# Kernel tuning notes

Measured on AMD Instinct MI355X. Metric: run time of the kernel, lower is better.

Reference implementation:

```python
import jax, jax.numpy as jnp
import numpy as np
from jax import lax

B, S, F, H, A, C = 256, 128, 128, 512, 512, 128


def _gru_cell(x, h, Wih, Whh, bih, bhh):
    # PyTorch GRU cell: gates ordered (r, z, n)
    gi = x @ Wih.T + bih            # [B, 3H]
    gh = h @ Whh.T + bhh            # [B, 3H]
    ir, iz, inn = jnp.split(gi, 3, axis=-1)
    hr, hz, hn = jnp.split(gh, 3, axis=-1)
    r = jax.nn.sigmoid(ir + hr)
    z = jax.nn.sigmoid(iz + hz)
    n = jnp.tanh(inn + r * hn)
    return (1.0 - z) * n + z * h


def setup_inputs() -> dict:
    key = jax.random.key(0)
    ks = jax.random.split(key, 13)
    def n(k, shape, s=0.05):
        return jax.random.normal(k, shape, dtype=jnp.float32) * s
    return dict(
        x=n(ks[0], (B, S, F), 1.0),
        y=jax.random.randint(ks[1], (B, C), 0, S),
        enc_Wih=n(ks[2], (3 * H, F)), enc_Whh=n(ks[3], (3 * H, H)),
        enc_bih=n(ks[4], (3 * H,)), enc_bhh=n(ks[5], (3 * H,)),
        dec_Wih=n(ks[6], (3 * H, F)), dec_Whh=n(ks[7], (3 * H, H)),
        dec_bih=n(ks[8], (3 * H,)), dec_bhh=n(ks[9], (3 * H,)),
        w1=n(ks[10], (A, H)), w2=n(ks[11], (A, H)), v=n(ks[12], (A,)),
    )


def reference(x, y, enc_Wih, enc_Whh, enc_bih, enc_bhh,
              dec_Wih, dec_Whh, dec_bih, dec_bhh, w1, w2, v):
    b, s, f = x.shape
    c = y.shape[1]
    h0 = jnp.zeros((b, H), x.dtype)

    # ---- encoder GRU over sequence ----
    def enc_step(h, xt):
        h2 = _gru_cell(xt, h, enc_Wih, enc_Whh, enc_bih, enc_bhh)
        return h2, h2
    hT, enc_out = lax.scan(enc_step, h0, jnp.swapaxes(x, 0, 1))  # enc_out [S,B,H]
    enc_out = jnp.swapaxes(enc_out, 0, 1)                        # [B,S,H]

    # w1(enc_out) is loop-invariant: precompute (same math as recomputing per step)
    enc_proj = jnp.einsum('bsh,ah->bsa', enc_out, w1)            # [B,S,A]

    # ---- decoder pointer loop (teacher_force_ratio=0.0 -> always use argmax) ----
    def dec_step(carry, y_i):
        h, dec_in = carry
        h = _gru_cell(dec_in, h, dec_Wih, dec_Whh, dec_bih, dec_bhh)  # [B,H]
        att = jax.nn.relu(enc_proj + (h @ w2.T)[:, None, :])          # [B,S,A]
        prob = jax.nn.softmax(jnp.einsum('bsa,a->bs', att, v), axis=1)  # [B,S]
        # faithful to original: F.cross_entropy applied to probabilities
        logp = jax.nn.log_softmax(prob, axis=1)
        step_loss = -jnp.mean(jnp.take_along_axis(logp, y_i[:, None], axis=1))
        pred = jnp.argmax(prob, axis=1)                               # [B]
        dec_in_next = jnp.take_along_axis(x, pred[:, None, None], axis=1)[:, 0, :]
        return (h, dec_in_next), (pred, step_loss)

    dec_in0 = jnp.zeros((b, f), x.dtype)
    (_, _), (preds, losses) = lax.scan(dec_step, (hT, dec_in0), y.T)
    preds = preds.T                                   # [B, C]
    loss = jnp.sum(losses) / b / c
    return preds, loss
```

## Files before the change

kernel.cpp:

```cpp
#include <hip/hip_runtime.h>
#include <math.h>

#define B_ 256
#define S_ 128
#define F_ 128
#define H_ 512
#define A_ 512
#define C_ 128

#define DOT4(va, vb) ((va).x*(vb).x + (va).y*(vb).y + (va).z*(vb).z + (va).w*(vb).w)

__global__ __launch_bounds__(256)
void transpose_x(const float* __restrict__ x, float* __restrict__ xT)
{
    const int t = blockIdx.x >> 2;
    const int f0 = (blockIdx.x & 3) * 32;
    const int b = threadIdx.x;
#pragma unroll 4
    for (int ff = 0; ff < 32; ++ff) {
        int f = f0 + ff;
        xT[(size_t)t * (F_ * B_) + (size_t)f * B_ + b] =
            x[(size_t)b * (S_ * F_) + (size_t)t * F_ + f];
    }
}

__global__ __launch_bounds__(256)
void prep_w6(const float* __restrict__ Wih, const float* __restrict__ Whh,
             float* __restrict__ W6)
{
    int id = blockIdx.x * 256 + threadIdx.x;
    if (id >= 256 * 640 * 6) return;
    int up = id / 3840;
    int rem = id - up * 3840;
    int k = rem / 6, g = rem - k * 6;
    int row = (g >> 1) * H_ + up * 2 + (g & 1);
    float val;
    if (k < F_) val = Wih[(size_t)row * F_ + k];
    else        val = Whh[(size_t)row * H_ + (k - F_)];
    W6[id] = val;
}

__global__ __launch_bounds__(256)
void prep_w2q(const float* __restrict__ w2, float4* __restrict__ w2q,
              float* __restrict__ dec_inT)
{
    int id = blockIdx.x * 256 + threadIdx.x;
    if (id < 128 * 512) {
        int k4 = id >> 9, a = id & 511;
        const float* s = w2 + (size_t)a * H_ + k4 * 4;
        w2q[id] = make_float4(s[0], s[1], s[2], s[3]);
    }
    if (id < F_ * B_) dec_inT[id] = 0.f;
}

__global__ __launch_bounds__(256)
void prep_bias(const float* __restrict__ ebih, const float* __restrict__ ebhh,
               const float* __restrict__ dbih, const float* __restrict__ dbhh,
               float* __restrict__ bias4e, float* __restrict__ bias4d,
               float* __restrict__ h0T)
{
    int id = blockIdx.x * 256 + threadIdx.x;
    if (id < H_ * B_) h0T[id] = 0.f;
    if (id < H_) {
        bias4e[id * 4 + 0] = ebih[id] + ebhh[id];
        bias4e[id * 4 + 1] = ebih[H_ + id] + ebhh[H_ + id];
        bias4e[id * 4 + 2] = ebih[2 * H_ + id];
        bias4e[id * 4 + 3] = ebhh[2 * H_ + id];
        bias4d[id * 4 + 0] = dbih[id] + dbhh[id];
        bias4d[id * 4 + 1] = dbih[H_ + id] + dbhh[H_ + id];
        bias4d[id * 4 + 2] = dbih[2 * H_ + id];
        bias4d[id * 4 + 3] = dbhh[2 * H_ + id];
    }
}

template<int NH>
__device__ __forceinline__ void acc_range(const float* __restrict__ src,
                                          const float* __restrict__ W6k,
                                          int nk, int b, float* __restrict__ acc)
{
    float a0[8], a1[8];
#pragma unroll
    for (int j = 0; j < 8; ++j) a0[j] = src[(size_t)j * B_ + b];
    for (int kc = 0; kc < nk; kc += 8) {
        if (kc + 8 < nk) {
#pragma unroll
            for (int j = 0; j < 8; ++j) a1[j] = src[(size_t)(kc + 8 + j) * B_ + b];
        }
        const float* Wr = W6k + (size_t)kc * 6;
#pragma unroll
        for (int j = 0; j < 8; ++j) {
            float av = a0[j];
            acc[0]      = fmaf(av, Wr[j * 6 + 0], acc[0]);
            acc[1]      = fmaf(av, Wr[j * 6 + 1], acc[1]);
            acc[2]      = fmaf(av, Wr[j * 6 + 2], acc[2]);
            acc[3]      = fmaf(av, Wr[j * 6 + 3], acc[3]);
            acc[NH]     = fmaf(av, Wr[j * 6 + 4], acc[NH]);
            acc[NH + 1] = fmaf(av, Wr[j * 6 + 5], acc[NH + 1]);
        }
#pragma unroll
        for (int j = 0; j < 8; ++j) a0[j] = a1[j];
    }
}

__global__ __launch_bounds__(512)
void gru_step(const float* __restrict__ inT,
              const float* __restrict__ hinT,
              const float* __restrict__ W6,
              const float* __restrict__ bias4,
              float* __restrict__ houtT,
              float* __restrict__ hB)
{
    __shared__ float accL[256][6];
    const int tid = threadIdx.x;
    const int lane = tid & 63;
    const int w = tid >> 6;
    const int bg = w & 3;
    const int kw = w >> 2;
    const int b = bg * 64 + lane;
    const int up = blockIdx.x;
    const float* Wb = W6 + (size_t)up * (640 * 6);

    float acc[8];
#pragma unroll
    for (int g = 0; g < 8; ++g) acc[g] = 0.f;

    if (kw == 0) {
        acc_range<4>(inT, Wb, F_, b, acc);
        acc_range<6>(hinT, Wb + F_ * 6, 192, b, acc);
    } else {
        acc_range<6>(hinT + (size_t)192 * B_, Wb + 320 * 6, 320, b, acc);
    }

    if (kw == 1) {
        const int li = tid & 255;
        accL[li][0] = acc[0]; accL[li][1] = acc[1];
        accL[li][2] = acc[2]; accL[li][3] = acc[3];
        accL[li][4] = acc[6]; accL[li][5] = acc[7];
    }
    __syncthreads();
    if (kw == 0) {
        const int u0 = up * 2, u1 = u0 + 1;
        float4 bb0 = *(const float4*)(bias4 + u0 * 4);
        float4 bb1 = *(const float4*)(bias4 + u1 * 4);
        float rr0 = 1.f / (1.f + expf(-(acc[0] + accL[tid][0] + bb0.x)));
        float rr1 = 1.f / (1.f + expf(-(acc[1] + accL[tid][1] + bb1.x)));
        float zz0 = 1.f / (1.f + expf(-(acc[2] + accL[tid][2] + bb0.y)));
        float zz1 = 1.f / (1.f + expf(-(acc[3] + accL[tid][3] + bb1.y)));
        float hn0 = acc[6] + accL[tid][4] + bb0.w;
        float hn1 = acc[7] + accL[tid][5] + bb1.w;
        float nn0 = tanhf(acc[4] + bb0.z + rr0 * hn0);
        float nn1 = tanhf(acc[5] + bb1.z + rr1 * hn1);
        float ho0 = hinT[(size_t)u0 * B_ + b];
        float ho1 = hinT[(size_t)u1 * B_ + b];
        float h0v = (1.f - zz0) * nn0 + zz0 * ho0;
        float h1v = (1.f - zz1) * nn1 + zz1 * ho1;
        houtT[(size_t)u0 * B_ + b] = h0v;
        houtT[(size_t)u1 * B_ + b] = h1v;
        if (hB) {
            hB[(size_t)b * H_ + u0] = h0v;
            hB[(size_t)b * H_ + u1] = h1v;
        }
    }
}

__global__ __launch_bounds__(512)
void w2attn_step(const float* __restrict__ hB,
                 const float4* __restrict__ w2q,
                 const float* __restrict__ v, const int* __restrict__ y,
                 int step, const float* __restrict__ x,
                 const float* __restrict__ proj,
                 float* __restrict__ dec_inT,
                 float* __restrict__ nlogp, float* __restrict__ preds_out)
{
    const int b = blockIdx.x;
    const int tid = threadIdx.x;
    __shared__ float sh[512];
    __shared__ float sq[512];
    __shared__ float sScore[S_], sProb[S_];
    __shared__ int sPred;

    sh[tid] = hB[(size_t)b * H_ + tid];
    __syncthreads();

    {
        float acc = 0.f;
        const float4* wp = w2q + tid;
#pragma unroll 8
        for (int k4 = 0; k4 < 128; ++k4) {
            float4 hv = *(const float4*)&sh[k4 * 4];
            float4 wv4 = wp[(size_t)k4 * 512];
            acc += DOT4(hv, wv4);
        }
        sq[tid] = acc;
    }
    __syncthreads();

    const int wv = tid >> 6, ln = tid & 63;
    float4 q0 = *(const float4*)&sq[ln * 8];
    float4 q1 = *(const float4*)&sq[ln * 8 + 4];
    float4 v0r = *(const float4*)(v + ln * 8);
    float4 v1r = *(const float4*)(v + ln * 8 + 4);
    const float* epb = proj + (size_t)b * (S_ * A_);
    for (int si = 0; si < 16; ++si) {
        int s = si * 8 + wv;
        const float* row = epb + (size_t)s * A_ + ln * 8;
        float4 p0 = *(const float4*)(row);
        float4 p1 = *(const float4*)(row + 4);
        float acc = fmaxf(p0.x + q0.x, 0.f) * v0r.x
                  + fmaxf(p0.y + q0.y, 0.f) * v0r.y
                  + fmaxf(p0.z + q0.z, 0.f) * v0r.z
                  + fmaxf(p0.w + q0.w, 0.f) * v0r.w
                  + fmaxf(p1.x + q1.x, 0.f) * v1r.x
                  + fmaxf(p1.y + q1.y, 0.f) * v1r.y
                  + fmaxf(p1.z + q1.z, 0.f) * v1r.z
                  + fmaxf(p1.w + q1.w, 0.f) * v1r.w;
#pragma unroll
        for (int off = 32; off; off >>= 1) acc += __shfl_down(acc, off);
        if (ln == 0) sScore[s] = acc;
    }
    __syncthreads();

    if (tid < 64) {
        float s0v = sScore[tid], s1v = sScore[tid + 64];
        float m = fmaxf(s0v, s1v);
#pragma unroll
        for (int off = 32; off; off >>= 1) m = fmaxf(m, __shfl_xor(m, off));
        float e0 = expf(s0v - m), e1 = expf(s1v - m);
        float se = e0 + e1;
#pragma unroll
        for (int off = 32; off; off >>= 1) se += __shfl_xor(se, off);
        float p0 = e0 / se, p1 = e1 / se;
        sProb[tid] = p0; sProb[tid + 64] = p1;
        float pm = fmaxf(p0, p1);
#pragma unroll
        for (int off = 32; off; off >>= 1) pm = fmaxf(pm, __shfl_xor(pm, off));
        float t0 = expf(p0 - pm), t1 = expf(p1 - pm);
        float T = t0 + t1;
#pragma unroll
        for (int off = 32; off; off >>= 1) T += __shfl_xor(T, off);
        float bv = p0; int bi2 = tid;
        if (p1 > bv) { bv = p1; bi2 = tid + 64; }
#pragma unroll
        for (int off = 32; off; off >>= 1) {
            float ov = __shfl_xor(bv, off);
            int oi = __shfl_xor(bi2, off);
            if (ov > bv || (ov == bv && oi < bi2)) { bv = ov; bi2 = oi; }
        }
        if (tid == 0) {
            sPred = bi2;
            int yy = y[(size_t)b * C_ + step];
            float py = sProb[yy];
            nlogp[(size_t)step * B_ + b] = -(py - pm - logf(T));
            preds_out[(size_t)b * C_ + step] = (float)bi2;
        }
    }
    __syncthreads();

    const int pred = sPred;
    if (tid < F_) {
        dec_inT[(size_t)tid * B_ + b] = x[((size_t)b * S_ + pred) * F_ + tid];
    }
}

__global__ __launch_bounds__(256)
void proj_gemm(const float* __restrict__ encT, const float* __restrict__ w1,
               float* __restrict__ proj)
{
    __shared__ float sA[32][128];
    __shared__ float sB[32][128];
    const int tid = threadIdx.x;
    const int s = blockIdx.z;
    const int b0 = blockIdx.y * 128;
    const int a0 = blockIdx.x * 128;
    const int tx = tid & 15, ty = tid >> 4;

    float acc[8][8];
#pragma unroll
    for (int i = 0; i < 8; ++i)
#pragma unroll
        for (int j = 0; j < 8; ++j) acc[i][j] = 0.f;

    const float* Abase = encT + (size_t)s * (H_ * B_) + b0;
    for (int kc = 0; kc < H_; kc += 32) {
#pragma unroll
        for (int p = 0; p < 16; ++p) {
            int idx = tid + p * 256;
            int kj = idx >> 7, bb = idx & 127;
            sA[kj][bb] = Abase[(size_t)(kc + kj) * B_ + bb];
        }
#pragma unroll
        for (int p = 0; p < 16; ++p) {
            int idx = tid + p * 256;
            int aa = idx >> 5, kj = idx & 31;
            sB[kj][aa] = w1[(size_t)(a0 + aa) * H_ + kc + kj];
        }
        __syncthreads();
#pragma unroll
        for (int kj = 0; kj < 32; ++kj) {
            float4 af0 = *(const float4*)&sA[kj][ty * 8];
            float4 af1 = *(const float4*)&sA[kj][ty * 8 + 4];
            float4 bf0 = *(const float4*)&sB[kj][tx * 8];
            float4 bf1 = *(const float4*)&sB[kj][tx * 8 + 4];
            float am[8] = {af0.x, af0.y, af0.z, af0.w, af1.x, af1.y, af1.z, af1.w};
            float bn[8] = {bf0.x, bf0.y, bf0.z, bf0.w, bf1.x, bf1.y, bf1.z, bf1.w};
#pragma unroll
            for (int i = 0; i < 8; ++i)
#pragma unroll
                for (int j = 0; j < 8; ++j)
                    acc[i][j] = fmaf(am[i], bn[j], acc[i][j]);
        }
        __syncthreads();
    }
#pragma unroll
    for (int i = 0; i < 8; ++i) {
        float* dst = proj + ((size_t)(b0 + ty * 8 + i) * S_ + s) * A_ + a0 + tx * 8;
        *(float4*)(dst) = make_float4(acc[i][0], acc[i][1], acc[i][2], acc[i][3]);
        *(float4*)(dst + 4) = make_float4(acc[i][4], acc[i][5], acc[i][6], acc[i][7]);
    }
}

__global__ void final_loss(const float* __restrict__ nlogp, float* __restrict__ out)
{
    __shared__ float part[C_];
    const int i = threadIdx.x;
    float s = 0.f;
    for (int b = 0; b < B_; ++b) s += nlogp[(size_t)i * B_ + b];
    part[i] = s / (float)B_;
    __syncthreads();
    if (i == 0) {
        float t = 0.f;
        for (int k = 0; k < C_; ++k) t += part[k];
        out[0] = t / (float)B_ / (float)C_;
    }
}

extern "C" void kernel_launch(void* const* d_in, const int* in_sizes, int n_in,
                              void* d_out, int out_size, void* d_ws, size_t ws_size,
                              hipStream_t stream)
{
    (void)in_sizes; (void)n_in; (void)out_size; (void)ws_size;
    const float* x    = (const float*)d_in[0];
    const int*   y    = (const int*)d_in[1];
    const float* eWih = (const float*)d_in[2];
    const float* eWhh = (const float*)d_in[3];
    const float* ebih = (const float*)d_in[4];
    const float* ebhh = (const float*)d_in[5];
    const float* dWih = (const float*)d_in[6];
    const float* dWhh = (const float*)d_in[7];
    const float* dbih = (const float*)d_in[8];
    const float* dbhh = (const float*)d_in[9];
    const float* w1   = (const float*)d_in[10];
    const float* w2   = (const float*)d_in[11];
    const float* v    = (const float*)d_in[12];
    float* out = (float*)d_out;

    float* ws = (float*)d_ws;
    float* encT    = ws;
    float* W6d     = ws;
    float* w2qf    = ws + 983040;
    float* hT0     = ws + 1245184;
    float* hT1     = ws + 1376256;
    float* dec_inT = ws + 1507328;
    float* nlogp   = ws + 1540096;
    float* hB      = ws + 1572864;
    float* encT127 = ws + 16646144;
    float* projB   = ws + 16777216;
    float* xT      = projB;
    float* W6e     = projB + 4194304;
    float* h0T     = projB + 5177344;
    float* bias4e  = ws + 33554432;
    float* bias4d  = ws + 33554432 + 2048;

    prep_bias<<<dim3(512), 256, 0, stream>>>(ebih, ebhh, dbih, dbhh,
                                             bias4e, bias4d, h0T);
    transpose_x<<<dim3(512), 256, 0, stream>>>(x, xT);
    prep_w6<<<dim3(3840), 256, 0, stream>>>(eWih, eWhh, W6e);

    for (int t = 0; t < S_; ++t) {
        const float* hin = (t == 0) ? h0T : encT + (size_t)(t - 1) * (H_ * B_);
        gru_step<<<dim3(256), 512, 0, stream>>>(
            xT + (size_t)t * (F_ * B_), hin, W6e, bias4e,
            encT + (size_t)t * (H_ * B_), (float*)nullptr);
    }

    proj_gemm<<<dim3(4, 2, 128), 256, 0, stream>>>(encT, w1, projB);

    prep_w6<<<dim3(3840), 256, 0, stream>>>(dWih, dWhh, W6d);
    prep_w2q<<<dim3(256), 256, 0, stream>>>(w2, (float4*)w2qf, dec_inT);

    float* hb[2] = { hT0, hT1 };
    for (int i = 0; i < C_; ++i) {
        const float* hin = (i == 0) ? encT127 : hb[(i & 1) ^ 1];
        float* hout = hb[i & 1];
        gru_step<<<dim3(256), 512, 0, stream>>>(dec_inT, hin, W6d, bias4d,
                                                hout, hB);
        w2attn_step<<<dim3(256), 512, 0, stream>>>(hB, (const float4*)w2qf, v, y,
                                                   i, x, projB, dec_inT,
                                                   nlogp, out);
    }

    final_loss<<<dim3(1), 128, 0, stream>>>(nlogp, out + (size_t)B_ * C_);
}
```

Baseline: 8.133 ms.

## Replace per-timestep encoder GRU launches with a persistent cooperative kernel

The 128 separate gru_step launches for the encoder are replaced by one cooperative persistent kernel. The kernel loops over timesteps and synchronises blocks through per-step atomic counters in global memory. Each block computes its input projection for step t before waiting on the flag, so part of the work overlaps the wait. This removes kernel launch overhead and the inter-launch gaps, at the cost of spin-waiting. Correctness depends on relaxed atomics and waitcnt giving cross-block visibility of the hidden state.

```diff
diff --git a/kernel.cpp b/kernel.cpp
--- a/kernel.cpp
+++ b/kernel.cpp
@@ -57,10 +57,11 @@
 void prep_bias(const float* __restrict__ ebih, const float* __restrict__ ebhh,
                const float* __restrict__ dbih, const float* __restrict__ dbhh,
                float* __restrict__ bias4e, float* __restrict__ bias4d,
-               float* __restrict__ h0T)
+               float* __restrict__ h0T, int* __restrict__ flags)
 {
     int id = blockIdx.x * 256 + threadIdx.x;
     if (id < H_ * B_) h0T[id] = 0.f;
+    if (id < S_) flags[id] = 0;
     if (id < H_) {
         bias4e[id * 4 + 0] = ebih[id] + ebhh[id];
         bias4e[id * 4 + 1] = ebih[H_ + id] + ebhh[H_ + id];
@@ -99,6 +100,88 @@
         }
 #pragma unroll
         for (int j = 0; j < 8; ++j) a0[j] = a1[j];
+    }
+}
+
+__global__ __launch_bounds__(512)
+void enc_persist(const float* __restrict__ xT,
+                 const float* __restrict__ W6,
+                 const float* __restrict__ bias4,
+                 const float* __restrict__ h0T,
+                 float* __restrict__ encT,
+                 int* __restrict__ flags)
+{
+    __shared__ float accL[256][6];
+    const int tid = threadIdx.x;
+    const int lane = tid & 63;
+    const int w = tid >> 6;
+    const int bg = w & 3;
+    const int kw = w >> 2;
+    const int b = bg * 64 + lane;
+    const int up = blockIdx.x;
+    const float* Wb = W6 + (size_t)up * (640 * 6);
+    const int u0 = up * 2, u1 = u0 + 1;
+    const float4 bb0 = *(const float4*)(bias4 + u0 * 4);
+    const float4 bb1 = *(const float4*)(bias4 + u1 * 4);
+
+    for (int t = 0; t < S_; ++t) {
+        const float* inT = xT + (size_t)t * (F_ * B_);
+        const float* hinT = (t == 0) ? h0T : encT + (size_t)(t - 1) * (H_ * B_);
+        float* houtT = encT + (size_t)t * (H_ * B_);
+
+        float acc[8];
+#pragma unroll
+        for (int g = 0; g < 8; ++g) acc[g] = 0.f;
+
+        if (kw == 0) acc_range<4>(inT, Wb, F_, b, acc);
+
+        if (t > 0) {
+            if (tid == 0) {
+                while (__hip_atomic_load(&flags[t - 1], __ATOMIC_RELAXED,
+                                         __HIP_MEMORY_SCOPE_AGENT) != 256) {
+                    __builtin_amdgcn_s_sleep(1);
+                }
+            }
+        }
+        __syncthreads();
+
+        if (kw == 0) {
+            acc_range<6>(hinT, Wb + F_ * 6, 192, b, acc);
+        } else {
+            acc_range<6>(hinT + (size_t)192 * B_, Wb + 320 * 6, 320, b, acc);
+        }
+
+        if (kw == 1) {
+            const int li = tid & 255;
+            accL[li][0] = acc[0]; accL[li][1] = acc[1];
+            accL[li][2] = acc[2]; accL[li][3] = acc[3];
+            accL[li][4] = acc[6]; accL[li][5] = acc[7];
+        }
+        __syncthreads();
+        if (kw == 0) {
+            float rr0 = 1.f / (1.f + expf(-(acc[0] + accL[tid][0] + bb0.x)));
+            float rr1 = 1.f / (1.f + expf(-(acc[1] + accL[tid][1] + bb1.x)));
+            float zz0 = 1.f / (1.f + expf(-(acc[2] + accL[tid][2] + bb0.y)));
+            float zz1 = 1.f / (1.f + expf(-(acc[3] + accL[tid][3] + bb1.y)));
+            float hn0 = acc[6] + accL[tid][4] + bb0.w;
+            float hn1 = acc[7] + accL[tid][5] + bb1.w;
+            float nn0 = tanhf(acc[4] + bb0.z + rr0 * hn0);
+            float nn1 = tanhf(acc[5] + bb1.z + rr1 * hn1);
+            float ho0 = hinT[(size_t)u0 * B_ + b];
+            float ho1 = hinT[(size_t)u1 * B_ + b];
+            float h0v = (1.f - zz0) * nn0 + zz0 * ho0;
+            float h1v = (1.f - zz1) * nn1 + zz1 * ho1;
+            __hip_atomic_store(&houtT[(size_t)u0 * B_ + b], h0v,
+                               __ATOMIC_RELAXED, __HIP_MEMORY_SCOPE_AGENT);
+            __hip_atomic_store(&houtT[(size_t)u1 * B_ + b], h1v,
+                               __ATOMIC_RELAXED, __HIP_MEMORY_SCOPE_AGENT);
+        }
+        asm volatile("s_waitcnt vmcnt(0)" ::: "memory");
+        __syncthreads();
+        if (tid == 0) {
+            __hip_atomic_fetch_add(&flags[t], 1, __ATOMIC_RELAXED,
+                                   __HIP_MEMORY_SCOPE_AGENT);
+        }
     }
 }
 
@@ -370,17 +453,18 @@
     float* h0T     = projB + 5177344;
     float* bias4e  = ws + 33554432;
     float* bias4d  = ws + 33554432 + 2048;
+    int*   flags   = (int*)(ws + 33554432 + 4096);
 
     prep_bias<<<dim3(512), 256, 0, stream>>>(ebih, ebhh, dbih, dbhh,
-                                             bias4e, bias4d, h0T);
+                                             bias4e, bias4d, h0T, flags);
     transpose_x<<<dim3(512), 256, 0, stream>>>(x, xT);
     prep_w6<<<dim3(3840), 256, 0, stream>>>(eWih, eWhh, W6e);
 
-    for (int t = 0; t < S_; ++t) {
-        const float* hin = (t == 0) ? h0T : encT + (size_t)(t - 1) * (H_ * B_);
-        gru_step<<<dim3(256), 512, 0, stream>>>(
-            xT + (size_t)t * (F_ * B_), hin, W6e, bias4e,
-            encT + (size_t)t * (H_ * B_), (float*)nullptr);
+    {
+        void* a[] = { (void*)&xT, (void*)&W6e, (void*)&bias4e, (void*)&h0T,
+                      (void*)&encT, (void*)&flags };
+        hipLaunchCooperativeKernel((const void*)enc_persist,
+                                   dim3(256), dim3(512), a, 0, stream);
     }
 
     proj_gemm<<<dim3(4, 2, 128), 256, 0, stream>>>(encT, w1, projB);
```

New measurement: 8.790 ms. 8.1% more time.

## Split GRU step across batch blocks, gather decoder input directly, merge prep kernels

Applied to the files above, without the earlier changes.

The GRU step kernel now runs 1024 blocks of 128 threads, with each block covering 64 batch rows for a unit pair, instead of 256 blocks of 512 threads. Its inner loop now prefetches 32 elements at a time instead of 8. The decoder input is no longer written transposed by the attention kernel. The GRU kernel instead reads x rows directly through a predicted-index buffer, and skips the input term on the first step. Prep kernels are merged into two launches, the workspace layout is reorganised, and the proj_gemm shared tile is padded. The aim is higher occupancy and less per-step launch and scatter overhead, at the cost of more register pressure from the 32-wide prefetch arrays.

```diff
diff --git a/kernel.cpp b/kernel.cpp
--- a/kernel.cpp
+++ b/kernel.cpp
@@ -7,59 +7,100 @@
 #define H_ 512
 #define A_ 512
 #define C_ 128
+#define HSLICE (H_ * B_)
 
 #define DOT4(va, vb) ((va).x*(vb).x + (va).y*(vb).y + (va).z*(vb).z + (va).w*(vb).w)
 
+template<int NH>
+__device__ __forceinline__ void acc_chunks(const float* __restrict__ src,
+                                           const float* __restrict__ W6k,
+                                           int nk, int b, float* __restrict__ acc)
+{
+    float a0[32], a1[32];
+#pragma unroll
+    for (int j = 0; j < 32; ++j) a0[j] = src[(size_t)j * B_ + b];
+    for (int kc = 0; kc < nk; kc += 32) {
+        if (kc + 32 < nk) {
+#pragma unroll
+            for (int j = 0; j < 32; ++j)
+                a1[j] = src[(size_t)(kc + 32 + j) * B_ + b];
+        }
+        const float* Wr = W6k + (size_t)kc * 6;
+#pragma unroll
+        for (int j = 0; j < 32; ++j) {
+            float av = a0[j];
+            acc[0]    = fmaf(av, Wr[j * 6 + 0], acc[0]);
+            acc[1]    = fmaf(av, Wr[j * 6 + 1], acc[1]);
+            acc[2]    = fmaf(av, Wr[j * 6 + 2], acc[2]);
+            acc[3]    = fmaf(av, Wr[j * 6 + 3], acc[3]);
+            acc[NH]   = fmaf(av, Wr[j * 6 + 4], acc[NH]);
+            acc[NH+1] = fmaf(av, Wr[j * 6 + 5], acc[NH + 1]);
+        }
+#pragma unroll
+        for (int j = 0; j < 32; ++j) a0[j] = a1[j];
+    }
+}
+
+__device__ __forceinline__ void acc_xrow(const float4* __restrict__ xr,
+                                         const float* __restrict__ W6k,
+                                         float* __restrict__ acc)
+{
+    float4 c0[8], c1[8];
+#pragma unroll
+    for (int j = 0; j < 8; ++j) c0[j] = xr[j];
+    for (int q = 0; q < 32; q += 8) {
+        if (q + 8 < 32) {
+#pragma unroll
+            for (int j = 0; j < 8; ++j) c1[j] = xr[q + 8 + j];
+        }
+#pragma unroll
+        for (int j = 0; j < 8; ++j) {
+            const float* Wr = W6k + (size_t)((q + j) * 4) * 6;
+            float e0 = c0[j].x, e1 = c0[j].y, e2 = c0[j].z, e3 = c0[j].w;
+#pragma unroll
+            for (int t2 = 0; t2 < 4; ++t2) {
+                float av = (t2 == 0) ? e0 : (t2 == 1) ? e1 : (t2 == 2) ? e2 : e3;
+                acc[0] = fmaf(av, Wr[t2 * 6 + 0], acc[0]);
+                acc[1] = fmaf(av, Wr[t2 * 6 + 1], acc[1]);
+                acc[2] = fmaf(av, Wr[t2 * 6 + 2], acc[2]);
+                acc[3] = fmaf(av, Wr[t2 * 6 + 3], acc[3]);
+                acc[4] = fmaf(av, Wr[t2 * 6 + 4], acc[4]);
+                acc[5] = fmaf(av, Wr[t2 * 6 + 5], acc[5]);
+            }
+        }
+#pragma unroll
+        for (int j = 0; j < 8; ++j) c0[j] = c1[j];
+    }
+}
+
 __global__ __launch_bounds__(256)
-void transpose_x(const float* __restrict__ x, float* __restrict__ xT)
-{
-    const int t = blockIdx.x >> 2;
-    const int f0 = (blockIdx.x & 3) * 32;
-    const int b = threadIdx.x;
-#pragma unroll 4
-    for (int ff = 0; ff < 32; ++ff) {
-        int f = f0 + ff;
-        xT[(size_t)t * (F_ * B_) + (size_t)f * B_ + b] =
-            x[(size_t)b * (S_ * F_) + (size_t)t * F_ + f];
-    }
-}
-
-__global__ __launch_bounds__(256)
-void prep_w6(const float* __restrict__ Wih, const float* __restrict__ Whh,
-             float* __restrict__ W6)
+void prep_all(const float* __restrict__ x,
+              const float* __restrict__ eWih, const float* __restrict__ eWhh,
+              const float* __restrict__ ebih, const float* __restrict__ ebhh,
+              const float* __restrict__ dbih, const float* __restrict__ dbhh,
+              float* __restrict__ xT, float* __restrict__ W6e,
+              float* __restrict__ bias4e, float* __restrict__ bias4d,
+              float* __restrict__ h0T)
 {
     int id = blockIdx.x * 256 + threadIdx.x;
-    if (id >= 256 * 640 * 6) return;
-    int up = id / 3840;
-    int rem = id - up * 3840;
-    int k = rem / 6, g = rem - k * 6;
-    int row = (g >> 1) * H_ + up * 2 + (g & 1);
-    float val;
-    if (k < F_) val = Wih[(size_t)row * F_ + k];
-    else        val = Whh[(size_t)row * H_ + (k - F_)];
-    W6[id] = val;
-}
-
-__global__ __launch_bounds__(256)
-void prep_w2q(const float* __restrict__ w2, float4* __restrict__ w2q,
-              float* __restrict__ dec_inT)
-{
-    int id = blockIdx.x * 256 + threadIdx.x;
-    if (id < 128 * 512) {
-        int k4 = id >> 9, a = id & 511;
-        const float* s = w2 + (size_t)a * H_ + k4 * 4;
-        w2q[id] = make_float4(s[0], s[1], s[2], s[3]);
-    }
-    if (id < F_ * B_) dec_inT[id] = 0.f;
-}
-
-__global__ __launch_bounds__(256)
-void prep_bias(const float* __restrict__ ebih, const float* __restrict__ ebhh,
-               const float* __restrict__ dbih, const float* __restrict__ dbhh,
-               float* __restrict__ bias4e, float* __restrict__ bias4d,
-               float* __restrict__ h0T)
-{
-    int id = blockIdx.x * 256 + threadIdx.x;
+    {
+        int up = id / 3840;
+        int rem = id - up * 3840;
+        int k = rem / 6, g = rem - k * 6;
+        int row = (g >> 1) * H_ + up * 2 + (g & 1);
+        float val;
+        if (k < F_) val = eWih[(size_t)row * F_ + k];
+        else        val = eWhh[(size_t)row * H_ + (k - F_)];
+        W6e[id] = val;
+    }
+#pragma unroll
+    for (int r = 0; r < 5; ++r) {
+        int xid = id + r * 983040;
+        if (xid < S_ * F_ * B_) {
+            int b2 = xid & 255, f = (xid >> 8) & 127, t = xid >> 15;
+            xT[xid] = x[(size_t)b2 * (S_ * F_) + (size_t)t * F_ + f];
+        }
+    }
     if (id < H_ * B_) h0T[id] = 0.f;
     if (id < H_) {
         bias4e[id * 4 + 0] = ebih[id] + ebhh[id];
@@ -73,87 +114,88 @@
     }
 }
 
-template<int NH>
-__device__ __forceinline__ void acc_range(const float* __restrict__ src,
-                                          const float* __restrict__ W6k,
-                                          int nk, int b, float* __restrict__ acc)
-{
-    float a0[8], a1[8];
-#pragma unroll
-    for (int j = 0; j < 8; ++j) a0[j] = src[(size_t)j * B_ + b];
-    for (int kc = 0; kc < nk; kc += 8) {
-        if (kc + 8 < nk) {
-#pragma unroll
-            for (int j = 0; j < 8; ++j) a1[j] = src[(size_t)(kc + 8 + j) * B_ + b];
-        }
-        const float* Wr = W6k + (size_t)kc * 6;
-#pragma unroll
-        for (int j = 0; j < 8; ++j) {
-            float av = a0[j];
-            acc[0]      = fmaf(av, Wr[j * 6 + 0], acc[0]);
-            acc[1]      = fmaf(av, Wr[j * 6 + 1], acc[1]);
-            acc[2]      = fmaf(av, Wr[j * 6 + 2], acc[2]);
-            acc[3]      = fmaf(av, Wr[j * 6 + 3], acc[3]);
-            acc[NH]     = fmaf(av, Wr[j * 6 + 4], acc[NH]);
-            acc[NH + 1] = fmaf(av, Wr[j * 6 + 5], acc[NH + 1]);
-        }
-#pragma unroll
-        for (int j = 0; j < 8; ++j) a0[j] = a1[j];
-    }
-}
-
-__global__ __launch_bounds__(512)
+__global__ __launch_bounds__(256)
+void prep_dec(const float* __restrict__ dWih, const float* __restrict__ dWhh,
+              const float* __restrict__ w2,
+              float* __restrict__ W6d, float4* __restrict__ w2q)
+{
+    int id = blockIdx.x * 256 + threadIdx.x;
+    {
+        int up = id / 3840;
+        int rem = id - up * 3840;
+        int k = rem / 6, g = rem - k * 6;
+        int row = (g >> 1) * H_ + up * 2 + (g & 1);
+        float val;
+        if (k < F_) val = dWih[(size_t)row * F_ + k];
+        else        val = dWhh[(size_t)row * H_ + (k - F_)];
+        W6d[id] = val;
+    }
+    if (id < 128 * 512) {
+        int k4 = id >> 9, a = id & 511;
+        const float* s = w2 + (size_t)a * H_ + k4 * 4;
+        w2q[id] = make_float4(s[0], s[1], s[2], s[3]);
+    }
+}
+
+__global__ __launch_bounds__(128)
 void gru_step(const float* __restrict__ inT,
+              const float* __restrict__ x,
+              const int*   __restrict__ pred,
               const float* __restrict__ hinT,
               const float* __restrict__ W6,
               const float* __restrict__ bias4,
               float* __restrict__ houtT,
               float* __restrict__ hB)
 {
-    __shared__ float accL[256][6];
+    __shared__ float accL[64][6];
     const int tid = threadIdx.x;
     const int lane = tid & 63;
-    const int w = tid >> 6;
-    const int bg = w & 3;
-    const int kw = w >> 2;
-    const int b = bg * 64 + lane;
-    const int up = blockIdx.x;
-    const float* Wb = W6 + (size_t)up * (640 * 6);
+    const int kw = tid >> 6;
+    const int up = blockIdx.x & 255;
+    const int bh = blockIdx.x >> 8;
+    const int b = bh * 64 + lane;
+    const float* Wb = W6 + (size_t)up * 3840;
+    const int u0 = up * 2, u1 = u0 + 1;
 
     float acc[8];
 #pragma unroll
     for (int g = 0; g < 8; ++g) acc[g] = 0.f;
 
+    float hold0 = 0.f, hold1 = 0.f;
     if (kw == 0) {
-        acc_range<4>(inT, Wb, F_, b, acc);
-        acc_range<6>(hinT, Wb + F_ * 6, 192, b, acc);
+        hold0 = hinT[(size_t)u0 * B_ + b];
+        hold1 = hinT[(size_t)u1 * B_ + b];
+        if (inT) {
+            acc_chunks<4>(inT, Wb, F_, b, acc);
+        } else if (pred) {
+            int pb = pred[b];
+            const float4* xr = (const float4*)(x + ((size_t)b * S_ + pb) * F_);
+            acc_xrow(xr, Wb, acc);
+        }
+        acc_chunks<6>(hinT, Wb + F_ * 6, 192, b, acc);
     } else {
-        acc_range<6>(hinT + (size_t)192 * B_, Wb + 320 * 6, 320, b, acc);
+        acc_chunks<6>(hinT + (size_t)192 * B_, Wb + 320 * 6, 320, b, acc);
     }
 
     if (kw == 1) {
-        const int li = tid & 255;
-        accL[li][0] = acc[0]; accL[li][1] = acc[1];
-        accL[li][2] = acc[2]; accL[li][3] = acc[3];
-        accL[li][4] = acc[6]; accL[li][5] = acc[7];
+        accL[lane][0] = acc[0]; accL[lane][1] = acc[1];
+        accL[lane][2] = acc[2]; accL[lane][3] = acc[3];
+        accL[lane][4] = acc[6]; accL[lane][5] = acc[7];
     }
     __syncthreads();
     if (kw == 0) {
-        const int u0 = up * 2, u1 = u0 + 1;
-        float4 bb0 = *(const float4*)(bias4 + u0 * 4);
-        float4 bb1 = *(const float4*)(bias4 + u1 * 4);
-        float rr0 = 1.f / (1.f + expf(-(acc[0] + accL[tid][0] + bb0.x)));
-        float rr1 = 1.f / (1.f + expf(-(acc[1] + accL[tid][1] + bb1.x)));
-        float zz0 = 1.f / (1.f + expf(-(acc[2] + accL[tid][2] + bb0.y)));
-        float zz1 = 1.f / (1.f + expf(-(acc[3] + accL[tid][3] + bb1.y)));
-        float hn0 = acc[6] + accL[tid][4] + bb0.w;
-        float hn1 = acc[7] + accL[tid][5] + bb1.w;
+        const float4 bb0 = *(const float4*)(bias4 + u0 * 4);
+        const float4 bb1 = *(const float4*)(bias4 + u1 * 4);
+        float rr0 = 1.f / (1.f + expf(-(acc[0] + accL[lane][0] + bb0.x)));
+        float rr1 = 1.f / (1.f + expf(-(acc[1] + accL[lane][1] + bb1.x)));
+        float zz0 = 1.f / (1.f + expf(-(acc[2] + accL[lane][2] + bb0.y)));
+        float zz1 = 1.f / (1.f + expf(-(acc[3] + accL[lane][3] + bb1.y)));
+        float hn0 = acc[6] + accL[lane][4] + bb0.w;
+        float hn1 = acc[7] + accL[lane][5] + bb1.w;
         float nn0 = tanhf(acc[4] + bb0.z + rr0 * hn0);
         float nn1 = tanhf(acc[5] + bb1.z + rr1 * hn1);
-        float ho0 = hinT[(size_t)u0 * B_ + b];
-        float ho1 = hinT[(size_t)u1 * B_ + b];
-        float h0v = (1.f - zz0) * nn0 + zz0 * ho0;
-        float h1v = (1.f - zz1) * nn1 + zz1 * ho1;
+        float h0v = (1.f - zz0) * nn0 + zz0 * hold0;
+        float h1v = (1.f - zz1) * nn1 + zz1 * hold1;
         houtT[(size_t)u0 * B_ + b] = h0v;
         houtT[(size_t)u1 * B_ + b] = h1v;
         if (hB) {
@@ -167,9 +209,8 @@
 void w2attn_step(const float* __restrict__ hB,
                  const float4* __restrict__ w2q,
                  const float* __restrict__ v, const int* __restrict__ y,
-                 int step, const float* __restrict__ x,
-                 const float* __restrict__ proj,
-                 float* __restrict__ dec_inT,
+                 int step, const float* __restrict__ proj,
+                 int* __restrict__ predBuf,
                  float* __restrict__ nlogp, float* __restrict__ preds_out)
 {
     const int b = blockIdx.x;
@@ -177,7 +218,6 @@
     __shared__ float sh[512];
     __shared__ float sq[512];
     __shared__ float sScore[S_], sProb[S_];
-    __shared__ int sPred;
 
     sh[tid] = hB[(size_t)b * H_ + tid];
     __syncthreads();
@@ -247,18 +287,12 @@
             if (ov > bv || (ov == bv && oi < bi2)) { bv = ov; bi2 = oi; }
         }
         if (tid == 0) {
-            sPred = bi2;
             int yy = y[(size_t)b * C_ + step];
             float py = sProb[yy];
             nlogp[(size_t)step * B_ + b] = -(py - pm - logf(T));
             preds_out[(size_t)b * C_ + step] = (float)bi2;
-        }
-    }
-    __syncthreads();
-
-    const int pred = sPred;
-    if (tid < F_) {
-        dec_inT[(size_t)tid * B_ + b] = x[((size_t)b * S_ + pred) * F_ + tid];
+            predBuf[b] = bi2;
+        }
     }
 }
 
@@ -267,7 +301,7 @@
                float* __restrict__ proj)
 {
     __shared__ float sA[32][128];
-    __shared__ float sB[32][128];
+    __shared__ float sB[32][132];
     const int tid = threadIdx.x;
     const int s = blockIdx.z;
     const int b0 = blockIdx.y * 128;
@@ -280,13 +314,13 @@
 #pragma unroll
         for (int j = 0; j < 8; ++j) acc[i][j] = 0.f;
 
-    const float* Abase = encT + (size_t)s * (H_ * B_) + b0;
+    const float* Abase = encT + (size_t)s * HSLICE + b0;
     for (int kc = 0; kc < H_; kc += 32) {
 #pragma unroll
         for (int p = 0; p < 16; ++p) {
             int idx = tid + p * 256;
-            int kj = idx >> 7, bb = idx & 127;
-            sA[kj][bb] = Abase[(size_t)(kc + kj) * B_ + bb];
+            int kj = idx >> 7, bbb = idx & 127;
+            sA[kj][bbb] = Abase[(size_t)(kc + kj) * B_ + bbb];
         }
 #pragma unroll
         for (int p = 0; p < 16; ++p) {
@@ -356,47 +390,46 @@
 
     float* ws = (float*)d_ws;
     float* encT    = ws;
-    float* W6d     = ws;
-    float* w2qf    = ws + 983040;
-    float* hT0     = ws + 1245184;
-    float* hT1     = ws + 1376256;
-    float* dec_inT = ws + 1507328;
-    float* nlogp   = ws + 1540096;
-    float* hB      = ws + 1572864;
-    float* encT127 = ws + 16646144;
-    float* projB   = ws + 16777216;
-    float* xT      = projB;
-    float* W6e     = projB + 4194304;
-    float* h0T     = projB + 5177344;
-    float* bias4e  = ws + 33554432;
-    float* bias4d  = ws + 33554432 + 2048;
-
-    prep_bias<<<dim3(512), 256, 0, stream>>>(ebih, ebhh, dbih, dbhh,
+    float* encT127 = ws + (size_t)127 * HSLICE;
+    float* projB  = ws + 16777216;
+    float* xT     = projB;
+    float* W6e    = projB + 4194304;
+    float* h0T    = projB + 5177344;
+    float* C0     = ws + 33554432;
+    float* bias4e = C0;
+    float* bias4d = C0 + 2048;
+    float* nlogp  = C0 + 4096;
+    float* hT0    = C0 + 36864;
+    float* hT1    = C0 + 167936;
+    float* hB     = C0 + 299008;
+    float* w2qf   = C0 + 430080;
+    float* W6d    = C0 + 692224;
+    int*   predBuf = (int*)(C0 + 1675264);
+
+    prep_all<<<dim3(3840), 256, 0, stream>>>(x, eWih, eWhh, ebih, ebhh,
+                                             dbih, dbhh, xT, W6e,
                                              bias4e, bias4d, h0T);
-    transpose_x<<<dim3(512), 256, 0, stream>>>(x, xT);
-    prep_w6<<<dim3(3840), 256, 0, stream>>>(eWih, eWhh, W6e);
 
     for (int t = 0; t < S_; ++t) {
-        const float* hin = (t == 0) ? h0T : encT + (size_t)(t - 1) * (H_ * B_);
-        gru_step<<<dim3(256), 512, 0, stream>>>(
-            xT + (size_t)t * (F_ * B_), hin, W6e, bias4e,
-            encT + (size_t)t * (H_ * B_), (float*)nullptr);
+        const float* hin = (t == 0) ? h0T : encT + (size_t)(t - 1) * HSLICE;
+        gru_step<<<dim3(1024), 128, 0, stream>>>(
+            xT + (size_t)t * (F_ * B_), nullptr, nullptr,
+            hin, W6e, bias4e, encT + (size_t)t * HSLICE, nullptr);
     }
 
     proj_gemm<<<dim3(4, 2, 128), 256, 0, stream>>>(encT, w1, projB);
 
-    prep_w6<<<dim3(3840), 256, 0, stream>>>(dWih, dWhh, W6d);
-    prep_w2q<<<dim3(256), 256, 0, stream>>>(w2, (float4*)w2qf, dec_inT);
+    prep_dec<<<dim3(3840), 256, 0, stream>>>(dWih, dWhh, w2, W6d, (float4*)w2qf);
 
     float* hb[2] = { hT0, hT1 };
-    for (int i = 0; i < C_; ++i) {
-        const float* hin = (i == 0) ? encT127 : hb[(i & 1) ^ 1];
-        float* hout = hb[i & 1];
-        gru_step<<<dim3(256), 512, 0, stream>>>(dec_inT, hin, W6d, bias4d,
-                                                hout, hB);
-        w2attn_step<<<dim3(256), 512, 0, stream>>>(hB, (const float4*)w2qf, v, y,
-                                                   i, x, projB, dec_inT,
-                                                   nlogp, out);
+    for (int st = 0; st < C_; ++st) {
+        const float* hin = (st == 0) ? encT127 : hb[(st & 1) ^ 1];
+        float* hout = hb[st & 1];
+        gru_step<<<dim3(1024), 128, 0, stream>>>(
+            nullptr, x, (st > 0) ? predBuf : nullptr,
+            hin, W6d, bias4d, hout, hB);
+        w2attn_step<<<dim3(256), 512, 0, stream>>>(
+            hB, (const float4*)w2qf, v, y, st, projB, predBuf, nlogp, out);
     }
 
     final_loss<<<dim3(1), 128, 0, stream>>>(nlogp, out + (size_t)B_ * C_);
```

After: 7.233 ms. -11.1%, faster.
